# Performance work log

Measured on AMD Instinct MI355X. Metric: run time of the kernel, lower is better.

## Reference

```python
import jax, jax.numpy as jnp
import numpy as np
import math

INPUT_SIZE = 1024
HIDDEN_SIZE = 1024
RANK = 256
BATCH = 32
SEQ = 512


def setup_inputs() -> dict:
    key = jax.random.key(0)
    k_x, k_a, k_b, k_c = jax.random.split(key, 4)
    stdv = 1.0 / math.sqrt(HIDDEN_SIZE)
    x = jax.random.normal(k_x, (BATCH, SEQ, INPUT_SIZE), dtype=jnp.float32)
    a = jax.random.uniform(k_a, (HIDDEN_SIZE, RANK * 4), minval=-stdv, maxval=stdv, dtype=jnp.float32)
    b = jax.random.uniform(k_b, (INPUT_SIZE, RANK * 4), minval=-stdv, maxval=stdv, dtype=jnp.float32)
    ct = jax.random.uniform(k_c, (RANK * 4, HIDDEN_SIZE), minval=-stdv, maxval=stdv, dtype=jnp.float32)
    return {"x": x, "a": a, "b": b, "ct": ct}


def reference(x, a, b, ct):
    B, S, _ = x.shape
    H = a.shape[0]
    R = a.shape[1] // 4
    ct3 = ct.reshape(4, R, H)  # (4, R, H)
    # Precompute input projection for all timesteps: (B, S, 4R)
    xb = jnp.einsum('bsi,ir->bsr', x, b)

    def step(carry, xb_t):
        h, c = carry
        g = (h @ a) * xb_t                      # (B, 4R)
        g = jnp.einsum('bkr,krh->bkh', g.reshape(B, 4, R), ct3)  # (B, 4, H)
        f_t = jax.nn.sigmoid(g[:, 0])
        i_t = jax.nn.sigmoid(g[:, 1])
        g_t = jnp.tanh(g[:, 2])
        o_t = jax.nn.sigmoid(g[:, 3])
        c = f_t * c + i_t * g_t
        h = o_t * jnp.tanh(c)
        return (h, c), h

    h0 = jnp.zeros((B, H), dtype=x.dtype)
    c0 = jnp.zeros((B, H), dtype=x.dtype)
    (h_t, c_t), hs = jax.lax.scan(step, (h0, c0), jnp.swapaxes(xb, 0, 1))
    hidden_seq = jnp.swapaxes(hs, 0, 1)  # (B, S, H)
    return hidden_seq, (h_t, c_t)
```

## Files before the change

kernel.cpp:

```cpp
#include <hip/hip_runtime.h>
#include <math.h>

#define NTHR 512
typedef unsigned long long u64;

__device__ __forceinline__ void st_uc(float* p, float v) {
    asm volatile("global_store_dword %0, %1, off sc0 sc1" :: "v"(p), "v"(v) : "memory");
}
#define LGKM0_BAR do { \
    asm volatile("s_waitcnt lgkmcnt(0)" ::: "memory"); \
    __builtin_amdgcn_s_barrier(); \
} while (0)

__global__ void init_kernel(u64* hp, u64* gp) {
    int i = blockIdx.x * blockDim.x + threadIdx.x;
    if (i < 65536) {
        __hip_atomic_store(hp + i, 0xFFFFFFFF00000000ull, __ATOMIC_RELAXED, __HIP_MEMORY_SCOPE_AGENT);
        __hip_atomic_store(gp + i, 0xFFFFFFFE00000000ull, __ATOMIC_RELAXED, __HIP_MEMORY_SCOPE_AGENT);
    }
}

__global__ __launch_bounds__(256) void xb_gemm(const float* __restrict__ X,
                                               const float* __restrict__ Bw,
                                               float* __restrict__ XB) {
    __shared__ float xs[16][132];
    __shared__ float bs[16][132];
    const int bm = blockIdx.x >> 3;
    const int bn = blockIdx.x & 7;
    const int m0 = bm * 128, n0 = bn * 128;
    const int tid = threadIdx.x;
    const int tx = tid & 15, ty = tid >> 4;
    float acc[8][8];
#pragma unroll
    for (int i = 0; i < 8; ++i)
#pragma unroll
        for (int j = 0; j < 8; ++j) acc[i][j] = 0.f;

    for (int k0 = 0; k0 < 1024; k0 += 16) {
#pragma unroll
        for (int p = 0; p < 2; ++p) {
            int f = tid + p * 256;
            int m = f >> 2, kq = f & 3;
            float4 v = *(const float4*)&X[(size_t)(m0 + m) * 1024 + k0 + kq * 4];
            xs[kq * 4 + 0][m] = v.x; xs[kq * 4 + 1][m] = v.y;
            xs[kq * 4 + 2][m] = v.z; xs[kq * 4 + 3][m] = v.w;
        }
#pragma unroll
        for (int p = 0; p < 2; ++p) {
            int f = tid + p * 256;
            int k = f >> 5, n = (f & 31) * 4;
            float4 v = *(const float4*)&Bw[(size_t)(k0 + k) * 1024 + n0 + n];
            *(float4*)&bs[k][n] = v;
        }
        __syncthreads();
#pragma unroll
        for (int k = 0; k < 16; ++k) {
            float xv[8], bv[8];
            *(float4*)&xv[0] = *(const float4*)&xs[k][ty * 8];
            *(float4*)&xv[4] = *(const float4*)&xs[k][ty * 8 + 4];
            *(float4*)&bv[0] = *(const float4*)&bs[k][tx * 8];
            *(float4*)&bv[4] = *(const float4*)&bs[k][tx * 8 + 4];
#pragma unroll
            for (int i = 0; i < 8; ++i)
#pragma unroll
                for (int j = 0; j < 8; ++j) acc[i][j] += xv[i] * bv[j];
        }
        __syncthreads();
    }
#pragma unroll
    for (int i = 0; i < 8; ++i)
#pragma unroll
        for (int j = 0; j < 8; j += 4) {
            float4 v = make_float4(acc[i][j], acc[i][j + 1], acc[i][j + 2], acc[i][j + 3]);
            *(float4*)&XB[(size_t)(m0 + ty * 8 + i) * 1024 + n0 + tx * 8 + j] = v;
        }
}

__global__ __launch_bounds__(NTHR, 1) void scan_kernel(
    const float* __restrict__ A, const float* __restrict__ CTm,
    float* __restrict__ XBH, u64* __restrict__ hp, u64* __restrict__ gp,
    float* __restrict__ ht_out, float* __restrict__ ct_out) {
    extern __shared__ float lds[];
    float* a_lf  = lds;
    float* ct_lf = lds + 16384;
    float* stgf  = lds + 32768;
    float* scr0  = lds + 36864;
    float* scr1  = lds + 37120;
    const float4* a_l4  = (const float4*)a_lf;
    const float4* ct_l4 = (const float4*)ct_lf;
    float4* stg4 = (float4*)stgf;

    const int wg  = blockIdx.x;
    const int bg0 = wg >> 6;
    const int bg1 = bg0 + 4;
    const int sg  = wg & 63;
    const int c0wg = sg * 16;
    const int tid = threadIdx.x;

    {
        const int c = tid & 15, i0 = tid >> 4;
        for (int i = i0; i < 1024; i += 32) {
            a_lf[c * 1024 + i]  = A[(size_t)i * 1024 + c0wg + c];
            ct_lf[c * 1024 + i] = CTm[(size_t)i * 1024 + c0wg + c];
        }
    }

    const int L  = tid & 63;
    const int w  = tid >> 6;
    const int Lc = L & 7;
    const int Lb = (L >> 3) & 3;
    const int cg = w & 1, kq = w >> 1;

    int wIdx[8], sIdx[4];
#pragma unroll
    for (int c = 0; c < 8; ++c) wIdx[c] = (cg * 8 + (c ^ Lc)) * 256 + kq * 64 + L;
#pragma unroll
    for (int r = 0; r < 4; ++r) sIdx[r] = ((r ^ Lb) << 8) + kq * 64 + L;

    const int e_b   = L >> 4;
    const int e_j   = L & 15;
    const int e_cgo = e_j >> 3;
    const int e_sx  = e_b * 8 + (e_j & 7);
    const int col   = c0wg + e_j;

    float creg = 0.f;
    float xbv  = 0.f;
    u64 qpf[8];

    auto issue_pf = [&](const u64* base) {
#pragma unroll
        for (int j = 0; j < 8; ++j)
            qpf[j] = __hip_atomic_load(base + tid + 512 * j, __ATOMIC_RELAXED,
                                       __HIP_MEMORY_SCOPE_AGENT);
    };

    auto compute = [&](const float4* wmat, float* scr) {
        float4 sv[4], wv[8];
#pragma unroll
        for (int r = 0; r < 4; ++r) sv[r] = stg4[sIdx[r]];
#pragma unroll
        for (int c = 0; c < 8; ++c) wv[c] = wmat[wIdx[c]];
        float v[32];
#pragma unroll
        for (int r = 0; r < 4; ++r)
#pragma unroll
            for (int c = 0; c < 8; ++c)
                v[r * 8 + c] = sv[r].x * wv[c].x + sv[r].y * wv[c].y
                             + sv[r].z * wv[c].z + sv[r].w * wv[c].w;
#pragma unroll
        for (int j = 0; j < 16; ++j) v[j] = v[2 * j] + __shfl_xor(v[2 * j + 1], 1);
#pragma unroll
        for (int j = 0; j < 8; ++j)  v[j] = v[2 * j] + __shfl_xor(v[2 * j + 1], 2);
#pragma unroll
        for (int j = 0; j < 4; ++j)  v[j] = v[2 * j] + __shfl_xor(v[2 * j + 1], 4);
#pragma unroll
        for (int j = 0; j < 2; ++j)  v[j] = v[2 * j] + __shfl_xor(v[2 * j + 1], 8);
        v[0] = v[0] + __shfl_xor(v[1], 16);
        v[0] = v[0] + __shfl_xor(v[0], 32);
        if (L < 32) scr[kq * 64 + cg * 32 + L] = v[0];
    };

    auto epiA_fn = [&](int t, const float* s, int bgx) {
        float q = s[e_cgo * 32 + e_sx] + s[64 + e_cgo * 32 + e_sx]
                + s[128 + e_cgo * 32 + e_sx] + s[192 + e_cgo * 32 + e_sx];
        u64 pk = ((u64)(unsigned)t << 32) | (u64)__float_as_uint(q * xbv);
        __hip_atomic_store(gp + (size_t)(t & 1) * 32768 + (size_t)(bgx * 4 + e_b) * 1024 + col,
                           pk, __ATOMIC_RELAXED, __HIP_MEMORY_SCOPE_AGENT);
    };
    auto epiB_fn = [&](int t, const float* s, int bgx) {
        float q0 = s[e_cgo * 32 + e_sx],       q1 = s[64 + e_cgo * 32 + e_sx];
        float q2 = s[128 + e_cgo * 32 + e_sx], q3 = s[192 + e_cgo * 32 + e_sx];
        float ft = 1.f / (1.f + __expf(-q0));
        float it = 1.f / (1.f + __expf(-q1));
        float gt = tanhf(q2);
        float ot = 1.f / (1.f + __expf(-q3));
        creg = ft * creg + it * gt;
        float hv = ot * tanhf(creg);
        int bglob = bgx * 4 + e_b;
        u64 pk = ((u64)(unsigned)t << 32) | (u64)__float_as_uint(hv);
        __hip_atomic_store(hp + (size_t)(t & 1) * 32768 + (size_t)bglob * 1024 + col,
                           pk, __ATOMIC_RELAXED, __HIP_MEMORY_SCOPE_AGENT);
        st_uc(XBH + ((size_t)bglob * 512 + t) * 1024 + col, hv);
        if (t == 511) {
            st_uc(ht_out + (size_t)bglob * 1024 + col, hv);
            st_uc(ct_out + (size_t)bglob * 1024 + col, creg);
        }
    };

    auto sub = [&](const u64* base, unsigned expect, const float4* wmat, float* scr,
                   int ek, int t, const u64* pfbase) {
        if (ek == 1) { if (w == 4 && t > 0) epiB_fn(t - 1, scr1, bg1); }
        else if (ek == 2) { if (w == 1) epiA_fn(t, scr0, bg0); }
        else if (ek == 3) { if (w == 2) epiA_fn(t, scr1, bg1); }
        else { if (w == 0) epiB_fn(t, scr0, bg0); }
        u64 q[8];
#pragma unroll
        for (int j = 0; j < 8; ++j) q[j] = qpf[j];
        for (;;) {
            bool ok = true;
#pragma unroll
            for (int j = 0; j < 8; ++j) ok &= ((unsigned)(q[j] >> 32) == expect);
            if (!__any(!ok)) break;
            __builtin_amdgcn_s_sleep(1);
#pragma unroll
            for (int j = 0; j < 8; ++j)
                q[j] = __hip_atomic_load(base + tid + 512 * j, __ATOMIC_RELAXED,
                                         __HIP_MEMORY_SCOPE_AGENT);
        }
#pragma unroll
        for (int j = 0; j < 8; ++j) stgf[tid + 512 * j] = __uint_as_float((unsigned)q[j]);
        LGKM0_BAR;
        issue_pf(pfbase);
        compute(wmat, scr);
        LGKM0_BAR;
    };

    __syncthreads();
    issue_pf(hp + 32768 + (size_t)bg0 * 4096);

    for (int k = 0; k < 512; ++k) {
        const unsigned expA = (unsigned)(k - 1);
        const unsigned expB = (unsigned)k;
        if (w == 1) xbv = __uint_as_float(__hip_atomic_load(
            (const unsigned*)(XBH + ((size_t)(bg0 * 4 + e_b) * 512 + k) * 1024 + col),
            __ATOMIC_RELAXED, __HIP_MEMORY_SCOPE_AGENT));
        if (w == 2) xbv = __uint_as_float(__hip_atomic_load(
            (const unsigned*)(XBH + ((size_t)(bg1 * 4 + e_b) * 512 + k) * 1024 + col),
            __ATOMIC_RELAXED, __HIP_MEMORY_SCOPE_AGENT));

        const size_t hsl = (size_t)((k + 1) & 1) * 32768;
        const size_t gsl = (size_t)(k & 1) * 32768;
        sub(hp + hsl + (size_t)bg0 * 4096, expA, a_l4, scr0, 1, k,
            hp + hsl + (size_t)bg1 * 4096);
        sub(hp + hsl + (size_t)bg1 * 4096, expA, a_l4, scr1, 2, k,
            gp + gsl + (size_t)bg0 * 4096);
        sub(gp + gsl + (size_t)bg0 * 4096, expB, ct_l4, scr0, 3, k,
            gp + gsl + (size_t)bg1 * 4096);
        sub(gp + gsl + (size_t)bg1 * 4096, expB, ct_l4, scr1, 4, k,
            hp + (size_t)(k & 1) * 32768 + (size_t)bg0 * 4096);
    }
    if (w == 4) epiB_fn(511, scr1, bg1);
}

extern "C" void kernel_launch(void* const* d_in, const int* in_sizes, int n_in,
                              void* d_out, int out_size, void* d_ws, size_t ws_size,
                              hipStream_t stream) {
    const float* X   = (const float*)d_in[0];
    const float* A   = (const float*)d_in[1];
    const float* Bw  = (const float*)d_in[2];
    const float* CTm = (const float*)d_in[3];

    float* out    = (float*)d_out;
    float* XBH    = out;
    float* ht_out = out + (size_t)32 * 512 * 1024;
    float* ct_out = ht_out + 32 * 1024;

    u64* hp = (u64*)d_ws;
    u64* gp = hp + 65536;

    (void)hipFuncSetAttribute((const void*)scan_kernel,
                              hipFuncAttributeMaxDynamicSharedMemorySize, 149504);

    init_kernel<<<dim3(256), dim3(256), 0, stream>>>(hp, gp);
    xb_gemm<<<dim3(1024), dim3(256), 0, stream>>>(X, Bw, XBH);
    scan_kernel<<<dim3(256), dim3(NTHR), 149504, stream>>>(A, CTm, XBH, hp, gp,
                                                           ht_out, ct_out);
}
```

Before: 4.580 ms.

## Process all 8 batch rows per stage instead of two interleaved half-batch groups

```diff
diff --git a/kernel.cpp b/kernel.cpp
--- a/kernel.cpp
+++ b/kernel.cpp
@@ -84,15 +84,13 @@
     float* a_lf  = lds;
     float* ct_lf = lds + 16384;
     float* stgf  = lds + 32768;
-    float* scr0  = lds + 36864;
-    float* scr1  = lds + 37120;
+    float* scrf  = stgf;
     const float4* a_l4  = (const float4*)a_lf;
     const float4* ct_l4 = (const float4*)ct_lf;
     float4* stg4 = (float4*)stgf;
 
     const int wg  = blockIdx.x;
-    const int bg0 = wg >> 6;
-    const int bg1 = bg0 + 4;
+    const int bg  = wg >> 6;
     const int sg  = wg & 63;
     const int c0wg = sg * 16;
     const int tid = threadIdx.x;
@@ -108,138 +106,128 @@
     const int L  = tid & 63;
     const int w  = tid >> 6;
     const int Lc = L & 7;
-    const int Lb = (L >> 3) & 3;
+    const int Lb = (L >> 3) & 7;
     const int cg = w & 1, kq = w >> 1;
 
-    int wIdx[8], sIdx[4];
+    int wIdx[8], sIdx[8];
 #pragma unroll
     for (int c = 0; c < 8; ++c) wIdx[c] = (cg * 8 + (c ^ Lc)) * 256 + kq * 64 + L;
 #pragma unroll
-    for (int r = 0; r < 4; ++r) sIdx[r] = ((r ^ Lb) << 8) + kq * 64 + L;
-
-    const int e_b   = L >> 4;
-    const int e_j   = L & 15;
-    const int e_cgo = e_j >> 3;
-    const int e_sx  = e_b * 8 + (e_j & 7);
+    for (int r = 0; r < 8; ++r) sIdx[r] = ((r ^ Lb) << 8) + kq * 64 + L;
+
+    const int scrpos = 64 * (L >> 3) + 32 * cg + 4 * (L & 7) + kq;
+
+    const int e_b   = tid >> 4;
+    const int e_j   = tid & 15;
     const int col   = c0wg + e_j;
+    const int bglob = bg * 8 + e_b;
 
     float creg = 0.f;
-    float xbv  = 0.f;
-    u64 qpf[8];
+    u64 qpf[16];
 
     auto issue_pf = [&](const u64* base) {
 #pragma unroll
-        for (int j = 0; j < 8; ++j)
-            qpf[j] = __hip_atomic_load(base + tid + 512 * j, __ATOMIC_RELAXED,
-                                       __HIP_MEMORY_SCOPE_AGENT);
+        for (int j = 0; j < 16; ++j)
+            qpf[j] = __hip_atomic_load(base + (j >> 2) * 2048 + 4 * tid + (j & 3),
+                                       __ATOMIC_RELAXED, __HIP_MEMORY_SCOPE_AGENT);
     };
-
-    auto compute = [&](const float4* wmat, float* scr) {
-        float4 sv[4], wv[8];
-#pragma unroll
-        for (int r = 0; r < 4; ++r) sv[r] = stg4[sIdx[r]];
+    auto validate_stage = [&](const u64* base, unsigned expect) {
+        for (;;) {
+            bool ok = true;
+#pragma unroll
+            for (int j = 0; j < 16; ++j) ok &= ((unsigned)(qpf[j] >> 32) == expect);
+            if (!__any(!ok)) break;
+            __builtin_amdgcn_s_sleep(1);
+#pragma unroll
+            for (int j = 0; j < 16; ++j)
+                qpf[j] = __hip_atomic_load(base + (j >> 2) * 2048 + 4 * tid + (j & 3),
+                                           __ATOMIC_RELAXED, __HIP_MEMORY_SCOPE_AGENT);
+        }
+#pragma unroll
+        for (int c = 0; c < 4; ++c) {
+            float4 f = make_float4(__uint_as_float((unsigned)qpf[4 * c]),
+                                   __uint_as_float((unsigned)qpf[4 * c + 1]),
+                                   __uint_as_float((unsigned)qpf[4 * c + 2]),
+                                   __uint_as_float((unsigned)qpf[4 * c + 3]));
+            stg4[c * 512 + tid] = f;
+        }
+    };
+    auto compute = [&](const float4* wmat) -> float {
+        float4 sv[8], wv[8];
+#pragma unroll
+        for (int r = 0; r < 8; ++r) sv[r] = stg4[sIdx[r]];
 #pragma unroll
         for (int c = 0; c < 8; ++c) wv[c] = wmat[wIdx[c]];
-        float v[32];
-#pragma unroll
-        for (int r = 0; r < 4; ++r)
+        float v[64];
+#pragma unroll
+        for (int r = 0; r < 8; ++r)
 #pragma unroll
             for (int c = 0; c < 8; ++c)
                 v[r * 8 + c] = sv[r].x * wv[c].x + sv[r].y * wv[c].y
                              + sv[r].z * wv[c].z + sv[r].w * wv[c].w;
 #pragma unroll
-        for (int j = 0; j < 16; ++j) v[j] = v[2 * j] + __shfl_xor(v[2 * j + 1], 1);
-#pragma unroll
-        for (int j = 0; j < 8; ++j)  v[j] = v[2 * j] + __shfl_xor(v[2 * j + 1], 2);
-#pragma unroll
-        for (int j = 0; j < 4; ++j)  v[j] = v[2 * j] + __shfl_xor(v[2 * j + 1], 4);
-#pragma unroll
-        for (int j = 0; j < 2; ++j)  v[j] = v[2 * j] + __shfl_xor(v[2 * j + 1], 8);
-        v[0] = v[0] + __shfl_xor(v[1], 16);
-        v[0] = v[0] + __shfl_xor(v[0], 32);
-        if (L < 32) scr[kq * 64 + cg * 32 + L] = v[0];
+        for (int j = 0; j < 32; ++j) v[j] = v[2 * j] + __shfl_xor(v[2 * j + 1], 1);
+#pragma unroll
+        for (int j = 0; j < 16; ++j) v[j] = v[2 * j] + __shfl_xor(v[2 * j + 1], 2);
+#pragma unroll
+        for (int j = 0; j < 8; ++j)  v[j] = v[2 * j] + __shfl_xor(v[2 * j + 1], 4);
+#pragma unroll
+        for (int j = 0; j < 4; ++j)  v[j] = v[2 * j] + __shfl_xor(v[2 * j + 1], 8);
+#pragma unroll
+        for (int j = 0; j < 2; ++j)  v[j] = v[2 * j] + __shfl_xor(v[2 * j + 1], 16);
+        return v[0] + __shfl_xor(v[1], 32);
     };
 
-    auto epiA_fn = [&](int t, const float* s, int bgx) {
-        float q = s[e_cgo * 32 + e_sx] + s[64 + e_cgo * 32 + e_sx]
-                + s[128 + e_cgo * 32 + e_sx] + s[192 + e_cgo * 32 + e_sx];
-        u64 pk = ((u64)(unsigned)t << 32) | (u64)__float_as_uint(q * xbv);
-        __hip_atomic_store(gp + (size_t)(t & 1) * 32768 + (size_t)(bgx * 4 + e_b) * 1024 + col,
-                           pk, __ATOMIC_RELAXED, __HIP_MEMORY_SCOPE_AGENT);
-    };
-    auto epiB_fn = [&](int t, const float* s, int bgx) {
-        float q0 = s[e_cgo * 32 + e_sx],       q1 = s[64 + e_cgo * 32 + e_sx];
-        float q2 = s[128 + e_cgo * 32 + e_sx], q3 = s[192 + e_cgo * 32 + e_sx];
-        float ft = 1.f / (1.f + __expf(-q0));
-        float it = 1.f / (1.f + __expf(-q1));
-        float gt = tanhf(q2);
-        float ot = 1.f / (1.f + __expf(-q3));
-        creg = ft * creg + it * gt;
-        float hv = ot * tanhf(creg);
-        int bglob = bgx * 4 + e_b;
-        u64 pk = ((u64)(unsigned)t << 32) | (u64)__float_as_uint(hv);
-        __hip_atomic_store(hp + (size_t)(t & 1) * 32768 + (size_t)bglob * 1024 + col,
-                           pk, __ATOMIC_RELAXED, __HIP_MEMORY_SCOPE_AGENT);
-        st_uc(XBH + ((size_t)bglob * 512 + t) * 1024 + col, hv);
-        if (t == 511) {
-            st_uc(ht_out + (size_t)bglob * 1024 + col, hv);
-            st_uc(ct_out + (size_t)bglob * 1024 + col, creg);
-        }
-    };
-
-    auto sub = [&](const u64* base, unsigned expect, const float4* wmat, float* scr,
-                   int ek, int t, const u64* pfbase) {
-        if (ek == 1) { if (w == 4 && t > 0) epiB_fn(t - 1, scr1, bg1); }
-        else if (ek == 2) { if (w == 1) epiA_fn(t, scr0, bg0); }
-        else if (ek == 3) { if (w == 2) epiA_fn(t, scr1, bg1); }
-        else { if (w == 0) epiB_fn(t, scr0, bg0); }
-        u64 q[8];
-#pragma unroll
-        for (int j = 0; j < 8; ++j) q[j] = qpf[j];
-        for (;;) {
-            bool ok = true;
-#pragma unroll
-            for (int j = 0; j < 8; ++j) ok &= ((unsigned)(q[j] >> 32) == expect);
-            if (!__any(!ok)) break;
-            __builtin_amdgcn_s_sleep(1);
-#pragma unroll
-            for (int j = 0; j < 8; ++j)
-                q[j] = __hip_atomic_load(base + tid + 512 * j, __ATOMIC_RELAXED,
-                                         __HIP_MEMORY_SCOPE_AGENT);
-        }
-#pragma unroll
-        for (int j = 0; j < 8; ++j) stgf[tid + 512 * j] = __uint_as_float((unsigned)q[j]);
-        LGKM0_BAR;
-        issue_pf(pfbase);
-        compute(wmat, scr);
-        LGKM0_BAR;
-    };
-
     __syncthreads();
-    issue_pf(hp + 32768 + (size_t)bg0 * 4096);
+    issue_pf(hp + 32768 + (size_t)bg * 8192);
 
     for (int k = 0; k < 512; ++k) {
-        const unsigned expA = (unsigned)(k - 1);
-        const unsigned expB = (unsigned)k;
-        if (w == 1) xbv = __uint_as_float(__hip_atomic_load(
-            (const unsigned*)(XBH + ((size_t)(bg0 * 4 + e_b) * 512 + k) * 1024 + col),
-            __ATOMIC_RELAXED, __HIP_MEMORY_SCOPE_AGENT));
-        if (w == 2) xbv = __uint_as_float(__hip_atomic_load(
-            (const unsigned*)(XBH + ((size_t)(bg1 * 4 + e_b) * 512 + k) * 1024 + col),
-            __ATOMIC_RELAXED, __HIP_MEMORY_SCOPE_AGENT));
-
         const size_t hsl = (size_t)((k + 1) & 1) * 32768;
         const size_t gsl = (size_t)(k & 1) * 32768;
-        sub(hp + hsl + (size_t)bg0 * 4096, expA, a_l4, scr0, 1, k,
-            hp + hsl + (size_t)bg1 * 4096);
-        sub(hp + hsl + (size_t)bg1 * 4096, expA, a_l4, scr1, 2, k,
-            gp + gsl + (size_t)bg0 * 4096);
-        sub(gp + gsl + (size_t)bg0 * 4096, expB, ct_l4, scr0, 3, k,
-            gp + gsl + (size_t)bg1 * 4096);
-        sub(gp + gsl + (size_t)bg1 * 4096, expB, ct_l4, scr1, 4, k,
-            hp + (size_t)(k & 1) * 32768 + (size_t)bg0 * 4096);
-    }
-    if (w == 4) epiB_fn(511, scr1, bg1);
+
+        float xbv = 0.f;
+        if (tid < 128) xbv = XBH[((size_t)bglob * 512 + k) * 1024 + col];
+
+        validate_stage(hp + hsl + (size_t)bg * 8192, (unsigned)(k - 1));
+        LGKM0_BAR;
+        float r = compute(a_l4);
+        issue_pf(gp + gsl + (size_t)bg * 8192);
+        LGKM0_BAR;
+        scrf[scrpos] = r;
+        LGKM0_BAR;
+        if (tid < 128) {
+            float4 sq = ((const float4*)scrf)[tid];
+            float gval = (sq.x + sq.y + sq.z + sq.w) * xbv;
+            u64 pk = ((u64)(unsigned)k << 32) | (u64)__float_as_uint(gval);
+            __hip_atomic_store(gp + gsl + (size_t)bglob * 1024 + col, pk,
+                               __ATOMIC_RELAXED, __HIP_MEMORY_SCOPE_AGENT);
+        }
+
+        validate_stage(gp + gsl + (size_t)bg * 8192, (unsigned)k);
+        LGKM0_BAR;
+        r = compute(ct_l4);
+        issue_pf(hp + gsl + (size_t)bg * 8192);
+        LGKM0_BAR;
+        scrf[scrpos] = r;
+        LGKM0_BAR;
+        if (tid < 128) {
+            float4 sq = ((const float4*)scrf)[tid];
+            float ft = 1.f / (1.f + __expf(-sq.x));
+            float it = 1.f / (1.f + __expf(-sq.y));
+            float gt = tanhf(sq.z);
+            float ot = 1.f / (1.f + __expf(-sq.w));
+            creg = ft * creg + it * gt;
+            float hv = ot * tanhf(creg);
+            u64 pk = ((u64)(unsigned)k << 32) | (u64)__float_as_uint(hv);
+            __hip_atomic_store(hp + gsl + (size_t)bglob * 1024 + col, pk,
+                               __ATOMIC_RELAXED, __HIP_MEMORY_SCOPE_AGENT);
+            st_uc(XBH + ((size_t)bglob * 512 + k) * 1024 + col, hv);
+            if (k == 511) {
+                st_uc(ht_out + (size_t)bglob * 1024 + col, hv);
+                st_uc(ct_out + (size_t)bglob * 1024 + col, creg);
+            }
+        }
+    }
 }
 
 extern "C" void kernel_launch(void* const* d_in, const int* in_sizes, int n_in,
@@ -259,10 +247,10 @@
     u64* gp = hp + 65536;
 
     (void)hipFuncSetAttribute((const void*)scan_kernel,
-                              hipFuncAttributeMaxDynamicSharedMemorySize, 149504);
+                              hipFuncAttributeMaxDynamicSharedMemorySize, 163840);
 
     init_kernel<<<dim3(256), dim3(256), 0, stream>>>(hp, gp);
     xb_gemm<<<dim3(1024), dim3(256), 0, stream>>>(X, Bw, XBH);
-    scan_kernel<<<dim3(256), dim3(NTHR), 149504, stream>>>(A, CTm, XBH, hp, gp,
+    scan_kernel<<<dim3(256), dim3(NTHR), 163840, stream>>>(A, CTm, XBH, hp, gp,
                                                            ht_out, ct_out);
 }
```

Result: slower. 9.325 ms (+103.6%).
